# Performance work log

Hardware: AMD Instinct MI355X
Metric: run time of the kernel (lower is better)

The kernel has to match this reference:

```python
import jax, jax.numpy as jnp
import numpy as np

N = 50000   # nodes per type (d and t)
E = 500000  # edges per relation
D = 128     # in = out features
NEG_SLOPE = 0.2


def setup_inputs() -> dict:
    key = jax.random.key(0)
    ks = jax.random.split(key, 24)
    s = 1.0 / np.sqrt(D)
    inp = {
        'x_d': jax.random.normal(ks[0], (N, D), jnp.float32),
        'x_t': jax.random.normal(ks[1], (N, D), jnp.float32),
        'W_dd': jax.random.normal(ks[2], (D, D), jnp.float32) * s,
        'W_tt': jax.random.normal(ks[3], (D, D), jnp.float32) * s,
        'W_dt': jax.random.normal(ks[4], (D, D), jnp.float32) * s,
        'al_dd': jax.random.normal(ks[5], (D,), jnp.float32) * s,
        'ar_dd': jax.random.normal(ks[6], (D,), jnp.float32) * s,
        'al_tt': jax.random.normal(ks[7], (D,), jnp.float32) * s,
        'ar_tt': jax.random.normal(ks[8], (D,), jnp.float32) * s,
        'al_dt': jax.random.normal(ks[9], (D,), jnp.float32) * s,
        'ar_dt': jax.random.normal(ks[10], (D,), jnp.float32) * s,
        'b_dd': jnp.zeros((D,), jnp.float32),
        'b_tt': jnp.zeros((D,), jnp.float32),
        'b_dt': jnp.zeros((D,), jnp.float32),
        'src_dd': jax.random.randint(ks[11], (E,), 0, N),
        'dst_dd': jax.random.randint(ks[12], (E,), 0, N),
        'src_tt': jax.random.randint(ks[13], (E,), 0, N),
        'dst_tt': jax.random.randint(ks[14], (E,), 0, N),
        'src_dt': jax.random.randint(ks[15], (E,), 0, N),
        'dst_dt': jax.random.randint(ks[16], (E,), 0, N),
        'src_td': jax.random.randint(ks[17], (E,), 0, N),
        'dst_td': jax.random.randint(ks[18], (E,), 0, N),
    }
    return inp


def _gat(x_src, x_dst, W, al, ar, b, src, dst, n_dst):
    """DGL GATConv (num_heads=1, no dropout, eval): gather -> edge attn ->
    per-destination segment softmax -> scatter-weighted aggregation + bias."""
    fs = x_src @ W                      # [Ns, D]
    fd = x_dst @ W                      # [Nd, D]
    el = fs @ al                        # [Ns]
    er = fd @ ar                        # [Nd]
    e = jax.nn.leaky_relu(el[src] + er[dst], NEG_SLOPE)   # [E]
    m = jax.ops.segment_max(e, dst, num_segments=n_dst)
    m = jnp.where(jnp.isfinite(m), m, jnp.float32(0))      # isolated dst nodes
    ex = jnp.exp(e - m[dst])
    ssum = jax.ops.segment_sum(ex, dst, num_segments=n_dst)
    alpha = ex / ssum[dst]              # [E]
    out = jax.ops.segment_sum(alpha[:, None] * fs[src], dst, num_segments=n_dst)
    return out + b


def reference(x_d, x_t, W_dd, W_tt, W_dt,
              al_dd, ar_dd, al_tt, ar_tt, al_dt, ar_dt,
              b_dd, b_tt, b_dt,
              src_dd, dst_dd, src_tt, dst_tt,
              src_dt, dst_dt, src_td, dst_td):
    # HeteroGraphConv with aggregate='sum'; 'dt' and 'td' share parameters.
    h_d = (_gat(x_d, x_d, W_dd, al_dd, ar_dd, b_dd, src_dd, dst_dd, N)
           + _gat(x_t, x_d, W_dt, al_dt, ar_dt, b_dt, src_td, dst_td, N))
    h_t = (_gat(x_t, x_t, W_tt, al_tt, ar_tt, b_tt, src_tt, dst_tt, N)
           + _gat(x_d, x_t, W_dt, al_dt, ar_dt, b_dt, src_dt, dst_dt, N))
    return jnp.stack([h_d, h_t])        # [2, N, D]
```

## Files before the change

### kernel.cpp

```cpp
#include <hip/hip_runtime.h>
#include <hip/hip_bf16.h>
#include <hip/hip_fp16.h>
#include <math.h>

#define DD 128
#define NEG_SLOPE 0.2f
#define CAP_B 2048
#define BSHIFT 7
#define MAXNB 512
#define NSCAT 160

typedef __attribute__((ext_vector_type(8))) short bf16x8;
typedef __attribute__((ext_vector_type(4))) float f32x4;
typedef __attribute__((ext_vector_type(8))) unsigned short u16x8;

__device__ __forceinline__ short f2bf(float f) {
    __hip_bfloat16 h = __float2bfloat16(f);
    return __builtin_bit_cast(short, h);
}
__device__ __forceinline__ float bf2f(unsigned short u) {
    return __uint_as_float(((unsigned)u) << 16);
}
__device__ __forceinline__ unsigned short f2h(float f) {
    return __builtin_bit_cast(unsigned short, __float2half(f));
}
__device__ __forceinline__ float h2f(unsigned short u) {
    return __half2float(__builtin_bit_cast(__half, u));
}
__device__ __forceinline__ float lrexp(float e) {
    e = (e > 0.f) ? e : NEG_SLOPE * e;
    return __expf(e);
}

__device__ __forceinline__ int permcol(int cp) { return (cp & 7) * 16 + (cp >> 3); }

__global__ __launch_bounds__(256) void pack_init_k(
    const float* __restrict__ W0, const float* __restrict__ W1,
    const float* __restrict__ W2,
    unsigned short* __restrict__ P0, unsigned short* __restrict__ P1,
    unsigned short* __restrict__ P2, int* __restrict__ cursor,
    const float* __restrict__ b_dd, const float* __restrict__ b_tt,
    const float* __restrict__ b_dt, float* __restrict__ pb0,
    float* __restrict__ pb1)
{
    if (blockIdx.x >= 24) {
        const int i = (blockIdx.x - 24) * 256 + threadIdx.x;
        if (i < 4 * MAXNB) cursor[i] = (i & (MAXNB - 1)) * CAP_B;
        if (blockIdx.x == 24) {
            const int t = threadIdx.x;
            if (t < 128) pb0[t] = b_dd[permcol(t)] + b_dt[permcol(t)];
            else         pb1[t - 128] = b_tt[permcol(t - 128)] + b_dt[permcol(t - 128)];
        }
        return;
    }
    const int t = blockIdx.x * 256 + threadIdx.x;
    const int m = t >> 11;
    const int r = t & 2047;
    const float* W = (m == 0) ? W0 : (m == 1) ? W1 : W2;
    unsigned short* P = (m == 0) ? P0 : (m == 1) ? P1 : P2;
    const int lane = r & 63;
    const int tile = r >> 6;
    const int ks = tile >> 3, ct = tile & 7;
    const int col = ct * 16 + (lane & 15);
    const int k0 = ks * 32 + (lane >> 4) * 8;
#pragma unroll
    for (int j = 0; j < 8; ++j)
        P[(size_t)r * 8 + j] = (unsigned short)f2bf(W[(size_t)(k0 + j) * DD + col]);
}

__device__ __forceinline__ void epi_store(
    f32x4 acc[8], const float* __restrict__ al, const float* __restrict__ ar,
    unsigned short* __restrict__ fb, float* __restrict__ el,
    float* __restrict__ er, int r0, int lane, int nrows)
{
    float pl[4] = {0.f, 0.f, 0.f, 0.f};
    float pr[4] = {0.f, 0.f, 0.f, 0.f};
#pragma unroll
    for (int ct = 0; ct < 8; ++ct) {
        const float alc = al[ct * 16 + (lane & 15)];
        const float arc = ar[ct * 16 + (lane & 15)];
#pragma unroll
        for (int g = 0; g < 4; ++g) {
            pl[g] = fmaf(acc[ct][g], alc, pl[g]);
            pr[g] = fmaf(acc[ct][g], arc, pr[g]);
        }
    }
#pragma unroll
    for (int o = 1; o < 16; o <<= 1) {
#pragma unroll
        for (int g = 0; g < 4; ++g) {
            pl[g] += __shfl_xor(pl[g], o, 16);
            pr[g] += __shfl_xor(pr[g], o, 16);
        }
    }
    if ((lane & 15) == 0) {
#pragma unroll
        for (int g = 0; g < 4; ++g) {
            const int r = r0 + (lane >> 4) * 4 + g;
            if (r < nrows) { el[r] = pl[g]; er[r] = pr[g]; }
        }
    }
#pragma unroll
    for (int g = 0; g < 4; ++g) {
        const int r = r0 + (lane >> 4) * 4 + g;
        if (r < nrows) {
            u16x8 v;
#pragma unroll
            for (int ct = 0; ct < 8; ++ct)
                v[ct] = (unsigned short)f2bf(acc[ct][g]);
            *((u16x8*)(fb + (size_t)r * DD + (lane & 15) * 8)) = v;
        }
    }
}

struct Prep5Args {
    const float* x[4];
    const unsigned short* Wp[4];
    const float* al[4]; const float* ar[4];
    unsigned short* fb[4]; float* el[4]; float* er[4];
    const int* src[4]; const int* dst[4];
    int* cursor; unsigned* ebuf;
    int n, nE, nb;
};

__global__ __launch_bounds__(512) void prep5_k(Prep5Args P)
{
    __shared__ unsigned short wlds[2048 * 8];

    const int v = blockIdx.y;
    if (v < 4) {
        const int lane = threadIdx.x & 63;
        const int wave = threadIdx.x >> 6;
        const int r0 = (blockIdx.x * 8 + wave) * 16;
        if (blockIdx.x * 128 >= P.n) return;

        const uint4* wsrc = (const uint4*)P.Wp[v];
        uint4* wdst = (uint4*)wlds;
#pragma unroll
        for (int i = 0; i < 4; ++i)
            wdst[threadIdx.x + i * 512] = wsrc[threadIdx.x + i * 512];
        __syncthreads();

        if (r0 >= P.n) return;
        const int arow = r0 + (lane & 15);
        const int arow_c = (arow < P.n) ? arow : (P.n - 1);
        const int kbase = (lane >> 4) * 8;
        const float* x = P.x[v];

        f32x4 acc[8];
#pragma unroll
        for (int ct = 0; ct < 8; ++ct) acc[ct] = (f32x4)(0.f);

#pragma unroll
        for (int ks = 0; ks < 4; ++ks) {
            const float* xp = x + (size_t)arow_c * DD + ks * 32 + kbase;
            const float4 a0 = ((const float4*)xp)[0];
            const float4 a1 = ((const float4*)xp)[1];
            bf16x8 af;
            af[0] = f2bf(a0.x); af[1] = f2bf(a0.y); af[2] = f2bf(a0.z); af[3] = f2bf(a0.w);
            af[4] = f2bf(a1.x); af[5] = f2bf(a1.y); af[6] = f2bf(a1.z); af[7] = f2bf(a1.w);
#pragma unroll
            for (int ct = 0; ct < 8; ++ct) {
                const bf16x8 w = *((const bf16x8*)(wlds + ((size_t)(ks * 8 + ct) * 64 + lane) * 8));
                acc[ct] = __builtin_amdgcn_mfma_f32_16x16x32_bf16(af, w, acc[ct], 0, 0, 0);
            }
        }
        epi_store(acc, P.al[v], P.ar[v], P.fb[v], P.el[v], P.er[v], r0, lane, P.n);
        return;
    }

    const int sb = blockIdx.x;
    if (sb >= 4 * NSCAT) return;
    int* cnt_s  = (int*)wlds;
    int* base_s = ((int*)wlds) + MAXNB;
    const int rel = sb / NSCAT;
    const int blk = sb - rel * NSCAT;
    const int* src = P.src[rel];
    const int* dst = P.dst[rel];
    int* cur = P.cursor + (size_t)rel * MAXNB;
    unsigned* eb = P.ebuf + (size_t)rel * P.nb * CAP_B;

    const int t = threadIdx.x;
    const int ch = (P.nE + NSCAT - 1) / NSCAT;
    const int i0 = blk * ch;
    const int i1 = (i0 + ch < P.nE) ? (i0 + ch) : P.nE;

    for (int i = t; i < MAXNB; i += 512) cnt_s[i] = 0;
    __syncthreads();
    for (int i = i0 + t; i < i1; i += 512)
        atomicAdd(&cnt_s[dst[i] >> BSHIFT], 1);
    __syncthreads();
    for (int b = t; b < P.nb; b += 512) {
        const int c = cnt_s[b];
        base_s[b] = c ? atomicAdd(cur + b, c) : 0;
        cnt_s[b] = 0;
    }
    __syncthreads();
    for (int i = i0 + t; i < i1; i += 512) {
        const int dv = dst[i];
        const int b = dv >> BSHIFT;
        const int p = base_s[b] + atomicAdd(&cnt_s[b], 1);
        eb[p] = ((unsigned)(dv & ((1 << BSHIFT) - 1)) << 16) | (unsigned)src[i];
    }
}

struct Sort2Args {
    const float* elA[2]; const float* erA[2];
    const float* elB[2]; const float* erB[2];
};

__global__ __launch_bounds__(256) void sort_alpha2_k(
    const unsigned* __restrict__ ebuf, const int* __restrict__ cursor,
    Sort2Args S, unsigned* __restrict__ cs32, int* __restrict__ rstart,
    int* __restrict__ rdeg, int n, int nb)
{
    const int b = blockIdx.x, ty = blockIdx.y, t = threadIdx.x;
    const int relA = ty;
    const int relB = ty ? 2 : 3;
    int cntA = cursor[(size_t)relA * MAXNB + b] - b * CAP_B;
    cntA = (cntA < 0) ? 0 : (cntA > CAP_B) ? CAP_B : cntA;
    int cntB = cursor[(size_t)relB * MAXNB + b] - b * CAP_B;
    cntB = (cntB < 0) ? 0 : (cntB > CAP_B) ? CAP_B : cntB;
    const int cnt = cntA + cntB;

    __shared__ unsigned buf[2 * CAP_B];
    __shared__ unsigned out32[2 * CAP_B];
    __shared__ int hist[128], off[128], cnt2[128], excl[128];
    __shared__ float ssumA[128], ssumB[128];
    __shared__ int total_s;

    const unsigned* ebA = ebuf + ((size_t)relA * nb + b) * CAP_B;
    const unsigned* ebB = ebuf + ((size_t)relB * nb + b) * CAP_B;
    for (int i = t; i < cntA; i += 256) buf[i] = ebA[i];
    for (int i = t; i < cntB; i += 256) buf[cntA + i] = ebB[i] | 0x80000000u;
    if (t < 128) { hist[t] = 0; cnt2[t] = 0; ssumA[t] = 0.f; ssumB[t] = 0.f; }
    __syncthreads();
    for (int i = t; i < cnt; i += 256) atomicAdd(&hist[(buf[i] >> 16) & 0x7f], 1);
    __syncthreads();
    if (t < 128) off[t] = (hist[t] + 3) & ~3;
    __syncthreads();
    for (int o = 1; o < 128; o <<= 1) {
        const int v = (t < 128 && t >= o) ? off[t - o] : 0;
        __syncthreads();
        if (t < 128) off[t] += v;
        __syncthreads();
    }
    if (t < 128) {
        const int pc = (hist[t] + 3) & ~3;
        excl[t] = off[t] - pc;
        const int d = b * 128 + t;
        if (d < n) {
            rstart[(size_t)ty * n + d] = b * (2 * CAP_B) + excl[t];
            rdeg[(size_t)ty * n + d] = pc;
        }
        for (int i = excl[t] + hist[t]; i < off[t]; ++i) out32[i] = 0u;
    }
    if (t == 127) total_s = off[127];
    __syncthreads();

    const float* elA = S.elA[ty]; const float* erA = S.erA[ty];
    const float* elB = S.elB[ty]; const float* erB = S.erB[ty];
    for (int i = t; i < cnt; i += 256) {
        const unsigned v = buf[i];
        const unsigned flag = v >> 31;
        const int local = (v >> 16) & 0x7f;
        const int s = v & 0xffffu;
        const int d = b * 128 + local;
        const float e = flag ? (elB[s] + erB[d]) : (elA[s] + erA[d]);
        const float ex = lrexp(e);
        atomicAdd(flag ? &ssumB[local] : &ssumA[local], ex);
        const int p = excl[local] + atomicAdd(&cnt2[local], 1);
        out32[p] = (unsigned)s | ((unsigned)f2h(ex) << 16) | (flag << 31);
    }
    __syncthreads();
    if (t < 128 && hist[t] > 0) {
        const float invA = (ssumA[t] > 0.f) ? 1.f / ssumA[t] : 0.f;
        const float invB = (ssumB[t] > 0.f) ? 1.f / ssumB[t] : 0.f;
        const int e0 = excl[t], e1 = excl[t] + hist[t];
        for (int i = e0; i < e1; ++i) {
            const unsigned v = out32[i];
            const unsigned flag = v >> 31;
            const float a = h2f((unsigned short)((v >> 16) & 0x7fff)) *
                            (flag ? invB : invA);
            out32[i] = (v & 0xffffu) | ((unsigned)f2h(a) << 16) | (flag << 31);
        }
    }
    __syncthreads();
    unsigned* cs = cs32 + ((size_t)ty * nb + b) * (2 * CAP_B);
    const int total = total_s;
    for (int i = t; i < total; i += 256) cs[i] = out32[i];
}

struct AggArgs {
    const int* rs; const int* rd;
    const unsigned* cs[2];
    const unsigned short* fbA[2];
    const unsigned short* fbB[2];
    const float* pb[2];
    float* out[2];
    int n;
};

__device__ __forceinline__ void fma8v(
    float a, const u16x8& v, float4& o0, float4& o1)
{
    o0.x = fmaf(a, bf2f(v[0]), o0.x);
    o0.y = fmaf(a, bf2f(v[1]), o0.y);
    o0.z = fmaf(a, bf2f(v[2]), o0.z);
    o0.w = fmaf(a, bf2f(v[3]), o0.w);
    o1.x = fmaf(a, bf2f(v[4]), o1.x);
    o1.y = fmaf(a, bf2f(v[5]), o1.y);
    o1.z = fmaf(a, bf2f(v[6]), o1.z);
    o1.w = fmaf(a, bf2f(v[7]), o1.w);
}

__global__ __launch_bounds__(256) void gat_aggregate_f(AggArgs A)
{
    const int lane = threadIdx.x & 15;
    const int grp  = threadIdx.x >> 4;
    const int gid = blockIdx.x * 16 + grp;
    if (gid >= 2 * A.n) return;
    const int ty = (gid >= A.n) ? 1 : 0;
    const int d = gid - ty * A.n;

    float4 o0 = ((const float4*)A.pb[ty])[lane * 2];
    float4 o1 = ((const float4*)A.pb[ty])[lane * 2 + 1];

    const unsigned short* fbA = A.fbA[ty];
    const unsigned short* fbB = A.fbB[ty];
    const int cnt = A.rd[(size_t)ty * A.n + d];
    if (cnt > 0) {
        const unsigned* csp = A.cs[ty] + A.rs[(size_t)ty * A.n + d];
        int k = 0;
        for (; k + 8 <= cnt; k += 8) {
            unsigned pv[8];
#pragma unroll
            for (int j = 0; j < 8; ++j) pv[j] = csp[k + j];
            u16x8 v[8];
#pragma unroll
            for (int j = 0; j < 8; ++j) {
                const unsigned short* fb = (pv[j] >> 31) ? fbB : fbA;
                v[j] = ((const u16x8*)(fb + (size_t)(pv[j] & 0xffffu) * DD))[lane];
            }
#pragma unroll
            for (int j = 0; j < 8; ++j)
                fma8v(h2f((unsigned short)((pv[j] >> 16) & 0x7fff)), v[j], o0, o1);
        }
        for (; k + 4 <= cnt; k += 4) {
            unsigned pv[4];
#pragma unroll
            for (int j = 0; j < 4; ++j) pv[j] = csp[k + j];
            u16x8 v[4];
#pragma unroll
            for (int j = 0; j < 4; ++j) {
                const unsigned short* fb = (pv[j] >> 31) ? fbB : fbA;
                v[j] = ((const u16x8*)(fb + (size_t)(pv[j] & 0xffffu) * DD))[lane];
            }
#pragma unroll
            for (int j = 0; j < 4; ++j)
                fma8v(h2f((unsigned short)((pv[j] >> 16) & 0x7fff)), v[j], o0, o1);
        }
    }

    float* op = A.out[ty] + (size_t)d * DD + lane;
    op[0]   = o0.x; op[16]  = o0.y; op[32]  = o0.z; op[48]  = o0.w;
    op[64]  = o1.x; op[80]  = o1.y; op[96]  = o1.z; op[112] = o1.w;
}

extern "C" void kernel_launch(void* const* d_in, const int* in_sizes, int n_in,
                              void* d_out, int out_size, void* d_ws, size_t ws_size,
                              hipStream_t stream)
{
    const float* x_d  = (const float*)d_in[0];
    const float* x_t  = (const float*)d_in[1];
    const float* W_dd = (const float*)d_in[2];
    const float* W_tt = (const float*)d_in[3];
    const float* W_dt = (const float*)d_in[4];
    const float* al_dd = (const float*)d_in[5];
    const float* ar_dd = (const float*)d_in[6];
    const float* al_tt = (const float*)d_in[7];
    const float* ar_tt = (const float*)d_in[8];
    const float* al_dt = (const float*)d_in[9];
    const float* ar_dt = (const float*)d_in[10];
    const float* b_dd  = (const float*)d_in[11];
    const float* b_tt  = (const float*)d_in[12];
    const float* b_dt  = (const float*)d_in[13];
    const int* src_dd = (const int*)d_in[14];
    const int* dst_dd = (const int*)d_in[15];
    const int* src_tt = (const int*)d_in[16];
    const int* dst_tt = (const int*)d_in[17];
    const int* src_dt = (const int*)d_in[18];
    const int* dst_dt = (const int*)d_in[19];
    const int* src_td = (const int*)d_in[20];
    const int* dst_td = (const int*)d_in[21];

    const int n  = in_sizes[0] / DD;
    const int nE = in_sizes[14];
    const int nb = (n + 127) >> BSHIFT;

    float* ws = (float*)d_ws;
    size_t off = 0;
    unsigned short* fb_dd   = (unsigned short*)(ws + off); off += (size_t)n * DD / 2;
    unsigned short* fb_tt   = (unsigned short*)(ws + off); off += (size_t)n * DD / 2;
    unsigned short* fb_dt_d = (unsigned short*)(ws + off); off += (size_t)n * DD / 2;
    unsigned short* fb_dt_t = (unsigned short*)(ws + off); off += (size_t)n * DD / 2;
    unsigned* ebuf = (unsigned*)(ws + off); off += (size_t)4 * nb * CAP_B;
    unsigned* cs32 = (unsigned*)(ws + off); off += (size_t)2 * nb * (2 * CAP_B);
    float* el_dd   = ws + off; off += n;
    float* er_dd   = ws + off; off += n;
    float* el_tt   = ws + off; off += n;
    float* er_tt   = ws + off; off += n;
    float* el_dt_d = ws + off; off += n;
    float* er_dt_d = ws + off; off += n;
    float* el_dt_t = ws + off; off += n;
    float* er_dt_t = ws + off; off += n;
    int* rstart = (int*)(ws + off); off += (size_t)2 * n;
    int* rdeg   = (int*)(ws + off); off += (size_t)2 * n;
    int* cursor = (int*)(ws + off); off += (size_t)4 * MAXNB;
    unsigned short* Wp_dd = (unsigned short*)(ws + off); off += 2048 * 8 / 2;
    unsigned short* Wp_tt = (unsigned short*)(ws + off); off += 2048 * 8 / 2;
    unsigned short* Wp_dt = (unsigned short*)(ws + off); off += 2048 * 8 / 2;
    float* pb0 = ws + off; off += DD;
    float* pb1 = ws + off; off += DD;

    if (ws_size < off * sizeof(float)) return;

    pack_init_k<<<32, 256, 0, stream>>>(W_dd, W_tt, W_dt, Wp_dd, Wp_tt, Wp_dt,
                                        cursor, b_dd, b_tt, b_dt, pb0, pb1);

    Prep5Args P;
    P.x[0] = x_d; P.x[1] = x_t; P.x[2] = x_d; P.x[3] = x_t;
    P.Wp[0] = Wp_dd; P.Wp[1] = Wp_tt; P.Wp[2] = Wp_dt; P.Wp[3] = Wp_dt;
    P.al[0] = al_dd; P.al[1] = al_tt; P.al[2] = al_dt; P.al[3] = al_dt;
    P.ar[0] = ar_dd; P.ar[1] = ar_tt; P.ar[2] = ar_dt; P.ar[3] = ar_dt;
    P.fb[0] = fb_dd; P.fb[1] = fb_tt; P.fb[2] = fb_dt_d; P.fb[3] = fb_dt_t;
    P.el[0] = el_dd; P.el[1] = el_tt; P.el[2] = el_dt_d; P.el[3] = el_dt_t;
    P.er[0] = er_dd; P.er[1] = er_tt; P.er[2] = er_dt_d; P.er[3] = er_dt_t;
    P.src[0] = src_dd; P.dst[0] = dst_dd;
    P.src[1] = src_tt; P.dst[1] = dst_tt;
    P.src[2] = src_dt; P.dst[2] = dst_dt;
    P.src[3] = src_td; P.dst[3] = dst_td;
    P.cursor = cursor; P.ebuf = ebuf;
    P.n = n; P.nE = nE; P.nb = nb;

    int gx = (n + 127) / 128;
    if (gx < 4 * NSCAT) gx = 4 * NSCAT;
    dim3 pgrid(gx, 5);
    prep5_k<<<pgrid, 512, 0, stream>>>(P);

    Sort2Args S;
    S.elA[0] = el_dd;   S.erA[0] = er_dd;
    S.elA[1] = el_tt;   S.erA[1] = er_tt;
    S.elB[0] = el_dt_t; S.erB[0] = er_dt_d;
    S.elB[1] = el_dt_d; S.erB[1] = er_dt_t;
    dim3 bgrid(nb, 2);
    sort_alpha2_k<<<bgrid, 256, 0, stream>>>(ebuf, cursor, S, cs32, rstart, rdeg, n, nb);

    AggArgs A;
    A.rs = rstart; A.rd = rdeg;
    A.cs[0] = cs32;
    A.cs[1] = cs32 + (size_t)nb * (2 * CAP_B);
    A.fbA[0] = fb_dd;   A.fbA[1] = fb_tt;
    A.fbB[0] = fb_dt_t; A.fbB[1] = fb_dt_d;
    A.pb[0] = pb0; A.pb[1] = pb1;
    A.out[0] = (float*)d_out;
    A.out[1] = (float*)d_out + (size_t)n * DD;
    A.n = n;

    const int aggrid = (2 * n + 15) / 16;
    gat_aggregate_f<<<aggrid, 256, 0, stream>>>(A);
}
```

Baseline: 151.6 us.

## Fuse segment softmax sort with aggregation using shared-memory edge lists

Merges the per-bucket sort/softmax kernel and the aggregation kernel into one kernel. Edge lists stay in LDS instead of being written to global memory with per-destination start/degree arrays. Relations A and B are kept in separate sublists, so the per-edge flag bit and feature-pointer select are removed. This removes a launch and a global round-trip, but aggregation parallelism drops to one block per 128-destination bucket, which may hurt latency hiding for the random feature gathers.

```diff
diff --git a/kernel.cpp b/kernel.cpp
--- a/kernel.cpp
+++ b/kernel.cpp
@@ -204,101 +204,14 @@
     }
 }
 
-struct Sort2Args {
+struct SortAggArgs {
     const float* elA[2]; const float* erA[2];
     const float* elB[2]; const float* erB[2];
-};
-
-__global__ __launch_bounds__(256) void sort_alpha2_k(
-    const unsigned* __restrict__ ebuf, const int* __restrict__ cursor,
-    Sort2Args S, unsigned* __restrict__ cs32, int* __restrict__ rstart,
-    int* __restrict__ rdeg, int n, int nb)
-{
-    const int b = blockIdx.x, ty = blockIdx.y, t = threadIdx.x;
-    const int relA = ty;
-    const int relB = ty ? 2 : 3;
-    int cntA = cursor[(size_t)relA * MAXNB + b] - b * CAP_B;
-    cntA = (cntA < 0) ? 0 : (cntA > CAP_B) ? CAP_B : cntA;
-    int cntB = cursor[(size_t)relB * MAXNB + b] - b * CAP_B;
-    cntB = (cntB < 0) ? 0 : (cntB > CAP_B) ? CAP_B : cntB;
-    const int cnt = cntA + cntB;
-
-    __shared__ unsigned buf[2 * CAP_B];
-    __shared__ unsigned out32[2 * CAP_B];
-    __shared__ int hist[128], off[128], cnt2[128], excl[128];
-    __shared__ float ssumA[128], ssumB[128];
-    __shared__ int total_s;
-
-    const unsigned* ebA = ebuf + ((size_t)relA * nb + b) * CAP_B;
-    const unsigned* ebB = ebuf + ((size_t)relB * nb + b) * CAP_B;
-    for (int i = t; i < cntA; i += 256) buf[i] = ebA[i];
-    for (int i = t; i < cntB; i += 256) buf[cntA + i] = ebB[i] | 0x80000000u;
-    if (t < 128) { hist[t] = 0; cnt2[t] = 0; ssumA[t] = 0.f; ssumB[t] = 0.f; }
-    __syncthreads();
-    for (int i = t; i < cnt; i += 256) atomicAdd(&hist[(buf[i] >> 16) & 0x7f], 1);
-    __syncthreads();
-    if (t < 128) off[t] = (hist[t] + 3) & ~3;
-    __syncthreads();
-    for (int o = 1; o < 128; o <<= 1) {
-        const int v = (t < 128 && t >= o) ? off[t - o] : 0;
-        __syncthreads();
-        if (t < 128) off[t] += v;
-        __syncthreads();
-    }
-    if (t < 128) {
-        const int pc = (hist[t] + 3) & ~3;
-        excl[t] = off[t] - pc;
-        const int d = b * 128 + t;
-        if (d < n) {
-            rstart[(size_t)ty * n + d] = b * (2 * CAP_B) + excl[t];
-            rdeg[(size_t)ty * n + d] = pc;
-        }
-        for (int i = excl[t] + hist[t]; i < off[t]; ++i) out32[i] = 0u;
-    }
-    if (t == 127) total_s = off[127];
-    __syncthreads();
-
-    const float* elA = S.elA[ty]; const float* erA = S.erA[ty];
-    const float* elB = S.elB[ty]; const float* erB = S.erB[ty];
-    for (int i = t; i < cnt; i += 256) {
-        const unsigned v = buf[i];
-        const unsigned flag = v >> 31;
-        const int local = (v >> 16) & 0x7f;
-        const int s = v & 0xffffu;
-        const int d = b * 128 + local;
-        const float e = flag ? (elB[s] + erB[d]) : (elA[s] + erA[d]);
-        const float ex = lrexp(e);
-        atomicAdd(flag ? &ssumB[local] : &ssumA[local], ex);
-        const int p = excl[local] + atomicAdd(&cnt2[local], 1);
-        out32[p] = (unsigned)s | ((unsigned)f2h(ex) << 16) | (flag << 31);
-    }
-    __syncthreads();
-    if (t < 128 && hist[t] > 0) {
-        const float invA = (ssumA[t] > 0.f) ? 1.f / ssumA[t] : 0.f;
-        const float invB = (ssumB[t] > 0.f) ? 1.f / ssumB[t] : 0.f;
-        const int e0 = excl[t], e1 = excl[t] + hist[t];
-        for (int i = e0; i < e1; ++i) {
-            const unsigned v = out32[i];
-            const unsigned flag = v >> 31;
-            const float a = h2f((unsigned short)((v >> 16) & 0x7fff)) *
-                            (flag ? invB : invA);
-            out32[i] = (v & 0xffffu) | ((unsigned)f2h(a) << 16) | (flag << 31);
-        }
-    }
-    __syncthreads();
-    unsigned* cs = cs32 + ((size_t)ty * nb + b) * (2 * CAP_B);
-    const int total = total_s;
-    for (int i = t; i < total; i += 256) cs[i] = out32[i];
-}
-
-struct AggArgs {
-    const int* rs; const int* rd;
-    const unsigned* cs[2];
     const unsigned short* fbA[2];
     const unsigned short* fbB[2];
     const float* pb[2];
     float* out[2];
-    int n;
+    int n, nb;
 };
 
 __device__ __forceinline__ void fma8v(
@@ -314,57 +227,149 @@
     o1.w = fmaf(a, bf2f(v[7]), o1.w);
 }
 
-__global__ __launch_bounds__(256) void gat_aggregate_f(AggArgs A)
-{
-    const int lane = threadIdx.x & 15;
-    const int grp  = threadIdx.x >> 4;
-    const int gid = blockIdx.x * 16 + grp;
-    if (gid >= 2 * A.n) return;
-    const int ty = (gid >= A.n) ? 1 : 0;
-    const int d = gid - ty * A.n;
-
-    float4 o0 = ((const float4*)A.pb[ty])[lane * 2];
-    float4 o1 = ((const float4*)A.pb[ty])[lane * 2 + 1];
-
+__global__ __launch_bounds__(256) void sortagg_k(
+    const unsigned* __restrict__ ebuf, const int* __restrict__ cursor,
+    SortAggArgs A)
+{
+    const int b = blockIdx.x, ty = blockIdx.y, t = threadIdx.x;
+    const int relA = ty;
+    const int relB = ty ? 2 : 3;
+    const int nb = A.nb;
+    int cntA = cursor[(size_t)relA * MAXNB + b] - b * CAP_B;
+    cntA = (cntA < 0) ? 0 : (cntA > CAP_B) ? CAP_B : cntA;
+    int cntB = cursor[(size_t)relB * MAXNB + b] - b * CAP_B;
+    cntB = (cntB < 0) ? 0 : (cntB > CAP_B) ? CAP_B : cntB;
+
+    __shared__ unsigned list[2 * CAP_B];
+    __shared__ int histA[128], histB[128], cnt2A[128], cnt2B[128];
+    __shared__ int offA[128], offB[128];
+    __shared__ float ssumA[128], ssumB[128];
+    __shared__ int totalA_s;
+
+    const unsigned* ebA = ebuf + ((size_t)relA * nb + b) * CAP_B;
+    const unsigned* ebB = ebuf + ((size_t)relB * nb + b) * CAP_B;
+
+    if (t < 128) { histA[t] = 0; histB[t] = 0; cnt2A[t] = 0; cnt2B[t] = 0;
+                   ssumA[t] = 0.f; ssumB[t] = 0.f; }
+    __syncthreads();
+    for (int i = t; i < cntA; i += 256) atomicAdd(&histA[ebA[i] >> 16], 1);
+    for (int i = t; i < cntB; i += 256) atomicAdd(&histB[ebB[i] >> 16], 1);
+    __syncthreads();
+    if (t < 128) {
+        offA[t] = (histA[t] + 3) & ~3;
+        offB[t] = (histB[t] + 3) & ~3;
+    }
+    __syncthreads();
+    for (int o = 1; o < 128; o <<= 1) {
+        int vA = 0, vB = 0;
+        if (t < 128 && t >= o) { vA = offA[t - o]; vB = offB[t - o]; }
+        __syncthreads();
+        if (t < 128) { offA[t] += vA; offB[t] += vB; }
+        __syncthreads();
+    }
+    if (t == 127) totalA_s = offA[127];
+    __syncthreads();
+    const int totalA = totalA_s;
+    if (t < 128) {
+        const int pcA = (histA[t] + 3) & ~3;
+        const int exA = offA[t] - pcA;
+        for (int i = exA + histA[t]; i < exA + pcA; ++i) list[i] = 0u;
+        const int pcB = (histB[t] + 3) & ~3;
+        const int exB = totalA + offB[t] - pcB;
+        for (int i = exB + histB[t]; i < exB + pcB; ++i) list[i] = 0u;
+    }
+    __syncthreads();
+
+    const float* elA = A.elA[ty]; const float* erA = A.erA[ty];
+    const float* elB = A.elB[ty]; const float* erB = A.erB[ty];
+    for (int i = t; i < cntA; i += 256) {
+        const unsigned v = ebA[i];
+        const int local = v >> 16;
+        const int s = v & 0xffffu;
+        const float ex = lrexp(elA[s] + erA[b * 128 + local]);
+        atomicAdd(&ssumA[local], ex);
+        const int pcA = (histA[local] + 3) & ~3;
+        const int p = (offA[local] - pcA) + atomicAdd(&cnt2A[local], 1);
+        list[p] = (unsigned)s | ((unsigned)f2h(ex) << 16);
+    }
+    for (int i = t; i < cntB; i += 256) {
+        const unsigned v = ebB[i];
+        const int local = v >> 16;
+        const int s = v & 0xffffu;
+        const float ex = lrexp(elB[s] + erB[b * 128 + local]);
+        atomicAdd(&ssumB[local], ex);
+        const int pcB = (histB[local] + 3) & ~3;
+        const int p = totalA + (offB[local] - pcB) + atomicAdd(&cnt2B[local], 1);
+        list[p] = (unsigned)s | ((unsigned)f2h(ex) << 16);
+    }
+    __syncthreads();
+    if (t < 128) {
+        if (histA[t] > 0) {
+            const float inv = 1.f / ssumA[t];
+            const int pcA = (histA[t] + 3) & ~3;
+            const int e0 = offA[t] - pcA, e1 = e0 + histA[t];
+            for (int i = e0; i < e1; ++i) {
+                const unsigned v = list[i];
+                const float a = h2f((unsigned short)(v >> 16)) * inv;
+                list[i] = (v & 0xffffu) | ((unsigned)f2h(a) << 16);
+            }
+        }
+        if (histB[t] > 0) {
+            const float inv = 1.f / ssumB[t];
+            const int pcB = (histB[t] + 3) & ~3;
+            const int e0 = totalA + offB[t] - pcB, e1 = e0 + histB[t];
+            for (int i = e0; i < e1; ++i) {
+                const unsigned v = list[i];
+                const float a = h2f((unsigned short)(v >> 16)) * inv;
+                list[i] = (v & 0xffffu) | ((unsigned)f2h(a) << 16);
+            }
+        }
+    }
+    __syncthreads();
+
+    const int lane = t & 15;
+    const int grp = t >> 4;
     const unsigned short* fbA = A.fbA[ty];
     const unsigned short* fbB = A.fbB[ty];
-    const int cnt = A.rd[(size_t)ty * A.n + d];
-    if (cnt > 0) {
-        const unsigned* csp = A.cs[ty] + A.rs[(size_t)ty * A.n + d];
-        int k = 0;
-        for (; k + 8 <= cnt; k += 8) {
-            unsigned pv[8];
-#pragma unroll
-            for (int j = 0; j < 8; ++j) pv[j] = csp[k + j];
-            u16x8 v[8];
-#pragma unroll
-            for (int j = 0; j < 8; ++j) {
-                const unsigned short* fb = (pv[j] >> 31) ? fbB : fbA;
-                v[j] = ((const u16x8*)(fb + (size_t)(pv[j] & 0xffffu) * DD))[lane];
-            }
-#pragma unroll
-            for (int j = 0; j < 8; ++j)
-                fma8v(h2f((unsigned short)((pv[j] >> 16) & 0x7fff)), v[j], o0, o1);
-        }
-        for (; k + 4 <= cnt; k += 4) {
+    for (int local = grp; local < 128; local += 16) {
+        const int d = b * 128 + local;
+        if (d >= A.n) continue;
+        float4 o0 = ((const float4*)A.pb[ty])[lane * 2];
+        float4 o1 = ((const float4*)A.pb[ty])[lane * 2 + 1];
+
+        const int pcA = (histA[local] + 3) & ~3;
+        const int exA = offA[local] - pcA;
+        for (int k = 0; k < pcA; k += 4) {
             unsigned pv[4];
 #pragma unroll
-            for (int j = 0; j < 4; ++j) pv[j] = csp[k + j];
+            for (int j = 0; j < 4; ++j) pv[j] = list[exA + k + j];
             u16x8 v[4];
 #pragma unroll
-            for (int j = 0; j < 4; ++j) {
-                const unsigned short* fb = (pv[j] >> 31) ? fbB : fbA;
-                v[j] = ((const u16x8*)(fb + (size_t)(pv[j] & 0xffffu) * DD))[lane];
-            }
-#pragma unroll
             for (int j = 0; j < 4; ++j)
-                fma8v(h2f((unsigned short)((pv[j] >> 16) & 0x7fff)), v[j], o0, o1);
-        }
-    }
-
-    float* op = A.out[ty] + (size_t)d * DD + lane;
-    op[0]   = o0.x; op[16]  = o0.y; op[32]  = o0.z; op[48]  = o0.w;
-    op[64]  = o1.x; op[80]  = o1.y; op[96]  = o1.z; op[112] = o1.w;
+                v[j] = ((const u16x8*)(fbA + (size_t)(pv[j] & 0xffffu) * DD))[lane];
+#pragma unroll
+            for (int j = 0; j < 4; ++j)
+                fma8v(h2f((unsigned short)(pv[j] >> 16)), v[j], o0, o1);
+        }
+        const int pcB = (histB[local] + 3) & ~3;
+        const int exB = totalA + offB[local] - pcB;
+        for (int k = 0; k < pcB; k += 4) {
+            unsigned pv[4];
+#pragma unroll
+            for (int j = 0; j < 4; ++j) pv[j] = list[exB + k + j];
+            u16x8 v[4];
+#pragma unroll
+            for (int j = 0; j < 4; ++j)
+                v[j] = ((const u16x8*)(fbB + (size_t)(pv[j] & 0xffffu) * DD))[lane];
+#pragma unroll
+            for (int j = 0; j < 4; ++j)
+                fma8v(h2f((unsigned short)(pv[j] >> 16)), v[j], o0, o1);
+        }
+
+        float* op = A.out[ty] + (size_t)d * DD + lane;
+        op[0]   = o0.x; op[16]  = o0.y; op[32]  = o0.z; op[48]  = o0.w;
+        op[64]  = o1.x; op[80]  = o1.y; op[96]  = o1.z; op[112] = o1.w;
+    }
 }
 
 extern "C" void kernel_launch(void* const* d_in, const int* in_sizes, int n_in,
@@ -405,7 +410,6 @@
     unsigned short* fb_dt_d = (unsigned short*)(ws + off); off += (size_t)n * DD / 2;
     unsigned short* fb_dt_t = (unsigned short*)(ws + off); off += (size_t)n * DD / 2;
     unsigned* ebuf = (unsigned*)(ws + off); off += (size_t)4 * nb * CAP_B;
-    unsigned* cs32 = (unsigned*)(ws + off); off += (size_t)2 * nb * (2 * CAP_B);
     float* el_dd   = ws + off; off += n;
     float* er_dd   = ws + off; off += n;
     float* el_tt   = ws + off; off += n;
@@ -414,8 +418,6 @@
     float* er_dt_d = ws + off; off += n;
     float* el_dt_t = ws + off; off += n;
     float* er_dt_t = ws + off; off += n;
-    int* rstart = (int*)(ws + off); off += (size_t)2 * n;
-    int* rdeg   = (int*)(ws + off); off += (size_t)2 * n;
     int* cursor = (int*)(ws + off); off += (size_t)4 * MAXNB;
     unsigned short* Wp_dd = (unsigned short*)(ws + off); off += 2048 * 8 / 2;
     unsigned short* Wp_tt = (unsigned short*)(ws + off); off += 2048 * 8 / 2;
@@ -448,25 +450,18 @@
     dim3 pgrid(gx, 5);
     prep5_k<<<pgrid, 512, 0, stream>>>(P);
 
-    Sort2Args S;
-    S.elA[0] = el_dd;   S.erA[0] = er_dd;
-    S.elA[1] = el_tt;   S.erA[1] = er_tt;
-    S.elB[0] = el_dt_t; S.erB[0] = er_dt_d;
-    S.elB[1] = el_dt_d; S.erB[1] = er_dt_t;
-    dim3 bgrid(nb, 2);
-    sort_alpha2_k<<<bgrid, 256, 0, stream>>>(ebuf, cursor, S, cs32, rstart, rdeg, n, nb);
-
-    AggArgs A;
-    A.rs = rstart; A.rd = rdeg;
-    A.cs[0] = cs32;
-    A.cs[1] = cs32 + (size_t)nb * (2 * CAP_B);
+    SortAggArgs A;
+    A.elA[0] = el_dd;   A.erA[0] = er_dd;
+    A.elA[1] = el_tt;   A.erA[1] = er_tt;
+    A.elB[0] = el_dt_t; A.erB[0] = er_dt_d;
+    A.elB[1] = el_dt_d; A.erB[1] = er_dt_t;
     A.fbA[0] = fb_dd;   A.fbA[1] = fb_tt;
     A.fbB[0] = fb_dt_t; A.fbB[1] = fb_dt_d;
     A.pb[0] = pb0; A.pb[1] = pb1;
     A.out[0] = (float*)d_out;
     A.out[1] = (float*)d_out + (size_t)n * DD;
-    A.n = n;
-
-    const int aggrid = (2 * n + 15) / 16;
-    gat_aggregate_f<<<aggrid, 256, 0, stream>>>(A);
-}
+    A.n = n; A.nb = nb;
+
+    dim3 agrid(nb, 2);
+    sortagg_k<<<agrid, 256, 0, stream>>>(ebuf, cursor, A);
+}
```

Result: no change. 152.4 us (+0.5%).
